# Optimization experiments

Hardware: AMD Instinct MI355X
Metric: run time of the kernel (lower is better)

Reference implementation:

```python
import jax, jax.numpy as jnp
import numpy as np

PI = np.pi
B, NLAT, NLON = 1, 91, 180
DIM, HEADS, DH, KM = 256, 8, 64, 3
DK = DH * KM          # 192: low-rank kernel head dim
LATD = 256            # latent_dim
NK_LONG, NK_LAT = 64, 32


def group_norm(x, g, w, b, eps=1e-5):
    # channel-last GroupNorm: normalize over (spatial..., channels-in-group) per sample
    bsz, C = x.shape[0], x.shape[-1]
    xg = x.reshape(bsz, -1, g, C // g)
    m = xg.mean(axis=(1, 3), keepdims=True)
    v = xg.var(axis=(1, 3), keepdims=True)
    xg = (xg - m) * jax.lax.rsqrt(v + eps)
    return xg.reshape(x.shape) * w + b


def layer_norm(x, w, b, eps=1e-5):
    m = x.mean(-1, keepdims=True)
    v = x.var(-1, keepdims=True)
    return (x - m) * jax.lax.rsqrt(v + eps) * w + b


def gated_mlp(x, w1, b1, w2, b2):
    # MLP([d, d, out], GeAct(GELU)): first linear doubled, gated GELU, then linear
    h = x @ w1 + b1
    c = h.shape[-1] // 2
    return (jax.nn.gelu(h[..., :c]) * h[..., c:]) @ w2 + b2


def pooling_reducer(x, mesh_w, win, lnw, lnb, w1, b1, w2, b2):
    # x: (b, n, m, c); optional mesh weighting along axis 1, mean over axis 2, PreNorm MLP
    x = x @ win
    if mesh_w is not None:
        x = x * mesh_w[None, :, None, None]
    x = x.mean(axis=tuple(range(2, x.ndim - 1)))
    return gated_mlp(layer_norm(x, lnw, lnb), w1, b1, w2, b2)


def bessel_mod(dist, freqs, weight, periodic):
    # radial Bessel basis: sqrt(2/c) * sin(f * d / c) / d, projected to (h, i, j, d)
    if periodic:
        dist = jnp.where(dist > PI, 2.0 * PI - dist, dist)
    d = dist[..., None] + 1e-5
    basis = np.float32(np.sqrt(2.0 / PI)) * jnp.sin(freqs * d / PI) / d  # (i, j, K)
    return jnp.einsum('ijk,khd->hijd', basis, weight)


def latitude_weights(lat, polar_eps=1.0):
    w = jnp.cos(lat)
    dlat = lat[1] - lat[0]
    pw = jnp.sin(dlat / 4.0) ** 2 / jnp.sin(dlat / 2.0)
    w = w.at[0].set(jnp.where(w[0] < 1e-3, polar_eps * pw, w[0]))
    w = w.at[-1].set(jnp.where(w[-1] < 1e-3, polar_eps * pw, w[-1]))
    return jax.lax.stop_gradient(w)  # cached/detached in the torch module


def low_rank_kernel(u_x, u_y, wk, mod):
    # project_qry=False: q is the raw query basis; scaling=1.0; leaky_relu applied outside softmax path
    b, nq, _ = u_x.shape
    nk = u_y.shape[1]
    q = u_x.reshape(b, nq, HEADS, DK).transpose(0, 2, 1, 3)
    k = (u_y @ wk).reshape(b, nk, HEADS, DK).transpose(0, 2, 1, 3)
    K = jnp.einsum('bhid,bhjd,hijd->bhij', q, k, mod)
    return jnp.where(K >= 0, K, 0.2 * K)  # leaky_relu(0.2)


def _forward(u_src, u_lat_qry, u_long_qry, src_lat, src_long, qry_lat, qry_long,
             cm_gn_w, cm_gn_b, cm_w1, cm_b1, cm_w2, cm_b2,
             tl_in_w, tl_ln_w, tl_ln_b, tl_w1, tl_b1, tl_w2, tl_b2,
             ta_in_w, ta_ln_w, ta_ln_b, ta_w1, ta_b1, ta_w2, ta_b2,
             klong_wk, klat_wk,
             pe_long_freq, pe_long_w, pe_lat_freq, pe_lat_w,
             mh_gn_w, mh_gn_b, mh_w):
    # channel mixer: GroupNorm(32) -> Linear -> GELU -> Linear, split into v and u
    u = group_norm(u_src, 32, cm_gn_w, cm_gn_b)
    u = jax.nn.gelu(u @ cm_w1 + cm_b1) @ cm_w2 + cm_b2
    v_src, u_mid = u[..., :HEADS * DH], u[..., HEADS * DH:]

    wlat = latitude_weights(src_lat)
    n_lat_src, n_lon_src = src_lat.shape[-1], src_long.shape[-1]

    # pooled reducers: long pools over lat; lat pools over lon with latitude weights
    u_long_src = pooling_reducer(jnp.swapaxes(u_mid, 1, 2), None,
                                 tl_in_w, tl_ln_w, tl_ln_b, tl_w1, tl_b1, tl_w2, tl_b2)
    u_lat_src = pooling_reducer(u_mid, wlat,
                                ta_in_w, ta_ln_w, ta_ln_b, ta_w1, ta_b1, ta_w2, ta_b2)

    # positional Bessel modulation (cached/detached distances in torch)
    long_dist = jax.lax.stop_gradient(jnp.abs(src_long[None, :] - qry_long[:, None]))
    lat_dist = jax.lax.stop_gradient(jnp.abs(src_lat[None, :] - qry_lat[:, None]))
    mod_long = bessel_mod(long_dist, pe_long_freq, pe_long_w, True)   # (h, lq, ls, DK)
    mod_lat = bessel_mod(lat_dist, pe_lat_freq, pe_lat_w, False)      # (h, iq, is, DK)

    k_long = low_rank_kernel(u_long_qry, u_long_src, klong_wk, mod_long)  # (b,h,lq,ls)
    k_lat = low_rank_kernel(u_lat_qry, u_lat_src, klat_wk, mod_lat)       # (b,h,iq,is)

    b, i, l, _ = v_src.shape
    u_phi = v_src.reshape(b, i, l, HEADS, DH).transpose(0, 3, 1, 2, 4)  # b h i l c
    k_lat = k_lat * wlat[None, None, None, :]
    u_phi = jnp.einsum('bhij,bhjmc->bhimc', k_lat, u_phi) * (PI / n_lat_src)
    u_phi = jnp.einsum('bhlm,bhimc->bhilc', k_long, u_phi) * (2.0 * PI / n_lon_src)
    bq, _, iq, lq, _ = u_phi.shape
    u_phi = u_phi.transpose(0, 2, 3, 1, 4).reshape(bq, iq, lq, HEADS * DH)
    return group_norm(u_phi, HEADS, mh_gn_w, mh_gn_b) @ mh_w


def setup_inputs() -> dict:
    keys = iter(jax.random.split(jax.random.key(0), 48))
    def rn(shape, scale=1.0):
        return jax.random.normal(next(keys), shape, dtype=jnp.float32) * scale
    d = {}
    d['u_src'] = rn((B, NLAT, NLON, DIM))
    d['u_lat_qry'] = rn((B, NLAT, HEADS * DK), 0.1)
    d['u_long_qry'] = rn((B, NLON, HEADS * DK), 0.1)
    lat = jnp.linspace(-PI / 2, PI / 2, NLAT, dtype=jnp.float32)  # includes poles
    lon = jnp.linspace(0.0, 2.0 * PI, NLON, endpoint=False, dtype=jnp.float32)
    d['src_lat'] = lat; d['qry_lat'] = lat
    d['src_long'] = lon; d['qry_long'] = lon
    d['cm_gn_w'] = jnp.ones((DIM,)); d['cm_gn_b'] = jnp.zeros((DIM,))
    d['cm_w1'] = rn((DIM, 4 * DIM), DIM ** -0.5); d['cm_b1'] = jnp.zeros((4 * DIM,))
    d['cm_w2'] = rn((4 * DIM, HEADS * DH + DIM), (4 * DIM) ** -0.5)
    d['cm_b2'] = jnp.zeros((HEADS * DH + DIM,))
    for p in ('tl', 'ta'):
        d[p + '_in_w'] = rn((DIM, DIM), DIM ** -0.5)
        d[p + '_ln_w'] = jnp.ones((DIM,)); d[p + '_ln_b'] = jnp.zeros((DIM,))
        d[p + '_w1'] = rn((DIM, 2 * DIM), DIM ** -0.5); d[p + '_b1'] = jnp.zeros((2 * DIM,))
        d[p + '_w2'] = rn((DIM, LATD), DIM ** -0.5); d[p + '_b2'] = jnp.zeros((LATD,))
    d['klong_wk'] = rn((LATD, HEADS * DK), LATD ** -0.5)
    d['klat_wk'] = rn((LATD, HEADS * DK), LATD ** -0.5)
    d['pe_long_freq'] = PI * jnp.arange(1, NK_LONG + 1, dtype=jnp.float32)
    d['pe_long_w'] = rn((NK_LONG, HEADS, DK), 0.02)
    d['pe_lat_freq'] = PI * jnp.arange(1, NK_LAT + 1, dtype=jnp.float32)
    d['pe_lat_w'] = rn((NK_LAT, HEADS, DK), 0.02)
    d['mh_gn_w'] = jnp.ones((HEADS * DH,)); d['mh_gn_b'] = jnp.zeros((HEADS * DH,))
    d['mh_w'] = rn((HEADS * DH, DIM), (HEADS * DH) ** -0.5)
    return d


def reference(u_src, u_lat_qry, u_long_qry, src_lat, src_long, qry_lat, qry_long,
              cm_gn_w, cm_gn_b, cm_w1, cm_b1, cm_w2, cm_b2,
              tl_in_w, tl_ln_w, tl_ln_b, tl_w1, tl_b1, tl_w2, tl_b2,
              ta_in_w, ta_ln_w, ta_ln_b, ta_w1, ta_b1, ta_w2, ta_b2,
              klong_wk, klat_wk,
              pe_long_freq, pe_long_w, pe_lat_freq, pe_lat_w,
              mh_gn_w, mh_gn_b, mh_w):
    return _forward(u_src, u_lat_qry, u_long_qry, src_lat, src_long, qry_lat, qry_long,
                    cm_gn_w, cm_gn_b, cm_w1, cm_b1, cm_w2, cm_b2,
                    tl_in_w, tl_ln_w, tl_ln_b, tl_w1, tl_b1, tl_w2, tl_b2,
                    ta_in_w, ta_ln_w, ta_ln_b, ta_w1, ta_b1, ta_w2, ta_b2,
                    klong_wk, klat_wk,
                    pe_long_freq, pe_long_w, pe_lat_freq, pe_lat_w,
                    mh_gn_w, mh_gn_b, mh_w)
```

## Files before the change

kernel.cpp:

```cpp
#include <hip/hip_runtime.h>
#include <math.h>

#define PI_F 3.14159265358979323846f

typedef __bf16  bf16x8  __attribute__((ext_vector_type(8)));
typedef float   floatx4 __attribute__((ext_vector_type(4)));

__device__ __forceinline__ float gelu_tanh(float x){
  float x3 = x*x*x;
  float t = tanhf(0.7978845608028654f*(x + 0.044715f*x3));
  return 0.5f*x*(1.0f+t);
}

__device__ __forceinline__ void gl_lds16(const void* g, void* l){
  __builtin_amdgcn_global_load_lds(
      (const __attribute__((address_space(1))) void*)(uintptr_t)g,
      (__attribute__((address_space(3))) void*)(uintptr_t)l,
      16, 0, 0);
}

__global__ __launch_bounds__(256) void prep_k(const float* __restrict__ w2in,
                                              __bf16* __restrict__ wt2,
                                              __bf16* __restrict__ kbuf,
                                              const float* __restrict__ lat,
                                              float* __restrict__ wlat){
  int b = blockIdx.x, t = threadIdx.x;
  if(b < 1440){
    int i = b*256 + t;
    if(i < 368640) kbuf[i] = (__bf16)0.f;
  } else if(b < 4512){
    int idx = (b-1440)*256 + t;
    int n = idx >> 10, k = idx & 1023;
    wt2[idx] = (__bf16)w2in[(size_t)k*768 + n];
  } else {
    if(t < 91) wlat[t] = cosf(lat[t]);
    __syncthreads();
    if(t == 0){
      float dlat = lat[1]-lat[0];
      float s4 = sinf(dlat*0.25f);
      float pw = s4*s4 / sinf(dlat*0.5f);
      if(wlat[0]  < 0.001f) wlat[0]  = pw;
      if(wlat[90] < 0.001f) wlat[90] = pw;
    }
  }
}

__global__ __launch_bounds__(256) void gn1cast_k(const float* __restrict__ x,
                                                 __bf16* __restrict__ xa,
                                                 float* __restrict__ part, int npos){
  int c = threadIdx.x;
  float s=0.f, q=0.f;
  for(int p=blockIdx.x; p<npos; p+=gridDim.x){
    float v = x[p*256 + c];
    xa[p*256 + c] = (__bf16)v;
    s += v; q += v*v;
  }
  __shared__ float ss[256], sq[256];
  ss[c]=s; sq[c]=q;
  __syncthreads();
  if((c&7)==0){
    float a=0.f,b=0.f;
    #pragma unroll
    for(int k=0;k<8;k++){ a+=ss[c+k]; b+=sq[c+k]; }
    int g=c>>3;
    part[(blockIdx.x*32+g)*2+0]=a;
    part[(blockIdx.x*32+g)*2+1]=b;
  }
}

__global__ __launch_bounds__(256) void gn_final_par(const float* __restrict__ part,
                                                    float* __restrict__ stats,
                                                    int nblk, float invN){
  int t = threadIdx.x;
  int g = t & 31, ch = t >> 5;
  float s=0.f,q=0.f;
  for(int b=ch; b<nblk; b+=8){
    s += part[(b*32+g)*2+0];
    q += part[(b*32+g)*2+1];
  }
  __shared__ float ss[256], sq[256];
  ss[t]=s; sq[t]=q;
  __syncthreads();
  if(t<32){
    float a=0.f,bq=0.f;
    #pragma unroll
    for(int c=0;c<8;c++){ a+=ss[c*32+t]; bq+=sq[c*32+t]; }
    float m = a*invN;
    float v = bq*invN - m*m;
    stats[t*2+0]=m;
    stats[t*2+1]=rsqrtf(v+1e-5f);
  }
}

__global__ __launch_bounds__(256) void w1fix_k(const float* __restrict__ w1,
                                               const float* __restrict__ b1,
                                               const float* __restrict__ stats,
                                               const float* __restrict__ gw,
                                               const float* __restrict__ gb,
                                               __bf16* __restrict__ wt1,
                                               float* __restrict__ b1p){
  int n = blockIdx.x, c = threadIdx.x;
  int g = c>>3;
  float m = stats[g*2+0], r = stats[g*2+1];
  float s = r*gw[c];
  float t = gb[c] - m*s;
  float w = w1[(size_t)c*1024 + n];
  wt1[(size_t)n*256 + c] = (__bf16)(s*w);
  __shared__ float red[256];
  red[c] = t*w; __syncthreads();
  for(int st=128; st>0; st>>=1){ if(c<st) red[c]+=red[c+st]; __syncthreads(); }
  if(c==0) b1p[n] = b1[n] + red[0];
}

__global__ __launch_bounds__(256) void w3fix_k(const float* __restrict__ mhw,
                                               const float* __restrict__ part2,
                                               const float* __restrict__ gw,
                                               const float* __restrict__ gb,
                                               __bf16* __restrict__ wt3,
                                               float* __restrict__ b3){
  __shared__ float st[16];
  __shared__ float ps[256], pq[256];
  int n = blockIdx.x, t = threadIdx.x;
  {
    int g = t & 7, ch = t >> 3;
    float s=0.f,q=0.f;
    for(int i=ch; i<91; i+=32){
      s += part2[(g*91+i)*2+0];
      q += part2[(g*91+i)*2+1];
    }
    ps[t]=s; pq[t]=q;
    __syncthreads();
    if(t<8){
      float a=0.f,bq=0.f;
      #pragma unroll
      for(int c=0;c<32;c++){ a+=ps[c*8+t]; bq+=pq[c*8+t]; }
      float m = a*(1.f/1048320.f);
      float v = bq*(1.f/1048320.f) - m*m;
      st[t*2+0]=m; st[t*2+1]=rsqrtf(v+1e-5f);
    }
    __syncthreads();
  }
  float bp=0.f;
  #pragma unroll
  for(int l=0;l<2;l++){
    int cc = t + l*256;
    int g = cc>>6;
    float m = st[g*2+0], r = st[g*2+1];
    float s = r*gw[cc];
    float tt = gb[cc] - m*s;
    float w = mhw[(size_t)cc*256 + n];
    wt3[(size_t)n*512 + cc] = (__bf16)(s*w);
    bp += tt*w;
  }
  __shared__ float red[256];
  red[t]=bp; __syncthreads();
  for(int stp=128;stp>0;stp>>=1){ if(t<stp) red[t]+=red[t+stp]; __syncthreads(); }
  if(t==0) b3[n]=red[0];
}

template<int ACT, int OUTMODE>
__global__ __launch_bounds__(256) void gemm_ld(const __bf16* __restrict__ A,
                                               const __bf16* __restrict__ Bt,
                                               const float* __restrict__ bias,
                                               void* __restrict__ Cp,
                                               __bf16* __restrict__ VB,
                                               __bf16* __restrict__ UM,
                                               int M, int N, int K)
{
  __shared__ __bf16 As[128][32];
  __shared__ __bf16 Bs[128][32];
  const int tid  = threadIdx.x;
  const int lane = tid & 63, wave = tid >> 6;
  const int row0 = blockIdx.x*128, col0 = blockIdx.y*128;
  const int lrow = lane >> 2;
  const int csw  = ((lane&3) ^ ((lane>>3)&3)) * 8;
  const int wr = (wave >> 1)*64, wc = (wave & 1)*64;
  const int m16 = lane & 15, quad = lane >> 4;
  const int pa = (quad ^ ((m16>>1)&3)) * 8;

  const __bf16* Ag0 = A  + (size_t)(row0 + wave*32 + lrow)*K + csw;
  const __bf16* Ag1 = Ag0 + (size_t)16*K;
  const __bf16* Bg0 = Bt + (size_t)(col0 + wave*32 + lrow)*K + csw;
  const __bf16* Bg1 = Bg0 + (size_t)16*K;
  void* la0 = &As[wave*32     ][0];
  void* la1 = &As[wave*32 + 16][0];
  void* lb0 = &Bs[wave*32     ][0];
  void* lb1 = &Bs[wave*32 + 16][0];

  floatx4 acc[4][4];
  #pragma unroll
  for(int i=0;i<4;i++)
    #pragma unroll
    for(int j=0;j<4;j++) acc[i][j] = (floatx4)0.f;

  const int kiters = K >> 5;
  for(int kk=0; kk<kiters; kk++){
    __syncthreads();
    gl_lds16(Ag0, la0);
    gl_lds16(Ag1, la1);
    gl_lds16(Bg0, lb0);
    gl_lds16(Bg1, lb1);
    Ag0 += 32; Ag1 += 32; Bg0 += 32; Bg1 += 32;
    __syncthreads();

    bf16x8 af[4], bfv[4];
    #pragma unroll
    for(int ti=0;ti<4;ti++) af[ti]  = *(const bf16x8*)&As[wr + ti*16 + m16][pa];
    #pragma unroll
    for(int tj=0;tj<4;tj++) bfv[tj] = *(const bf16x8*)&Bs[wc + tj*16 + m16][pa];
    #pragma unroll
    for(int ti=0;ti<4;ti++)
      #pragma unroll
      for(int tj=0;tj<4;tj++)
        acc[ti][tj] = __builtin_amdgcn_mfma_f32_16x16x32_bf16(af[ti], bfv[tj], acc[ti][tj], 0,0,0);
  }

  #pragma unroll
  for(int ti=0;ti<4;ti++){
    #pragma unroll
    for(int reg=0;reg<4;reg++){
      int gr = row0 + wr + ti*16 + quad*4 + reg;
      if(gr >= M) continue;
      int jj = gr/180, mm = gr - jj*180;
      #pragma unroll
      for(int tj=0;tj<4;tj++){
        int gc = col0 + wc + tj*16 + m16;
        float v = acc[ti][tj][reg];
        if(bias) v += bias[gc];
        if(ACT==1) v = gelu_tanh(v);
        if(OUTMODE==2){
          if(gc < 512){
            int hh = gc>>6, cc = gc&63;
            VB[(((size_t)(hh*180+mm)*91)+jj)*64 + cc] = (__bf16)v;
          } else {
            UM[(size_t)gr*256 + (gc-512)] = (__bf16)v;
          }
        } else if(OUTMODE==1){
          ((__bf16*)Cp)[(size_t)gr*N + gc] = (__bf16)v;
        } else {
          ((float*)Cp)[(size_t)gr*N + gc]  = v;
        }
      }
    }
  }
}

__global__ __launch_bounds__(256) void means_k(const __bf16* __restrict__ um,
                                               float* __restrict__ mlon_axis,
                                               float* __restrict__ mlat_axis){
  int b = blockIdx.x, c = threadIdx.x;
  if(b < 180){
    float s=0.f;
    for(int j=0;j<91;j++) s += (float)um[(size_t)(j*180+b)*256 + c];
    mlon_axis[b*256+c] = s*(1.0f/91.0f);
  } else {
    int latr = b-180;
    const __bf16* base = um + (size_t)latr*180*256 + c;
    float s=0.f;
    for(int m=0;m<180;m++) s += (float)base[(size_t)m*256];
    mlat_axis[latr*256+c] = s*(1.0f/180.0f);
  }
}

__device__ __forceinline__ void pool_body(int r, int t,
    const float* __restrict__ x, const float* __restrict__ rs,
    const float* __restrict__ inw,
    const float* __restrict__ lnw, const float* __restrict__ lnb,
    const float* __restrict__ w1, const float* __restrict__ b1,
    const float* __restrict__ w2, const float* __restrict__ b2,
    float* __restrict__ out,
    float* xs, float* xn, float* red, float* g){
  xs[t] = x[r*256+t];
  __syncthreads();
  float y=0.f;
  for(int c=0;c<256;c++) y += xs[c]*inw[c*256+t];
  if(rs) y *= rs[r];
  red[t]=y; __syncthreads();
  for(int s=128;s>0;s>>=1){ if(t<s) red[t]+=red[t+s]; __syncthreads(); }
  float m = red[0]*(1.f/256.f); __syncthreads();
  float d = y-m; red[t]=d*d; __syncthreads();
  for(int s=128;s>0;s>>=1){ if(t<s) red[t]+=red[t+s]; __syncthreads(); }
  float var = red[0]*(1.f/256.f);
  __syncthreads();
  xn[t] = d*rsqrtf(var+1e-5f)*lnw[t]+lnb[t];
  __syncthreads();
  float s1=b1[t], s2=b1[256+t];
  for(int c=0;c<256;c++){ float xv=xn[c]; s1 += xv*w1[c*512+t]; s2 += xv*w1[c*512+256+t]; }
  g[t] = gelu_tanh(s1)*s2;
  __syncthreads();
  float o=b2[t];
  for(int c=0;c<256;c++) o += g[c]*w2[c*256+t];
  out[r*256+t]=o;
}

__global__ __launch_bounds__(256) void pool2_k(
    const float* __restrict__ mlon_axis, const float* __restrict__ mlat_axis,
    const float* __restrict__ wlat,
    const float* __restrict__ tl_inw, const float* __restrict__ tl_lnw, const float* __restrict__ tl_lnb,
    const float* __restrict__ tl_w1, const float* __restrict__ tl_b1,
    const float* __restrict__ tl_w2, const float* __restrict__ tl_b2,
    const float* __restrict__ ta_inw, const float* __restrict__ ta_lnw, const float* __restrict__ ta_lnb,
    const float* __restrict__ ta_w1, const float* __restrict__ ta_b1,
    const float* __restrict__ ta_w2, const float* __restrict__ ta_b2,
    float* __restrict__ ulsrc, float* __restrict__ uasrc){
  __shared__ float xs[256], xn[256], red[256], g[256];
  int b = blockIdx.x, t = threadIdx.x;
  if(b < 180)
    pool_body(b, t, mlon_axis, nullptr, tl_inw, tl_lnw, tl_lnb, tl_w1, tl_b1, tl_w2, tl_b2,
              ulsrc, xs, xn, red, g);
  else
    pool_body(b-180, t, mlat_axis, wlat, ta_inw, ta_lnw, ta_lnb, ta_w1, ta_b1, ta_w2, ta_b2,
              uasrc, xs, xn, red, g);
}

__global__ __launch_bounds__(256) void rowmmT2_k(const float* __restrict__ ulsrc,
                                                 const float* __restrict__ uasrc,
                                                 const float* __restrict__ wlong,
                                                 const float* __restrict__ wlatk,
                                                 float* __restrict__ klkl,
                                                 float* __restrict__ klka){
  int b = blockIdx.x, t = threadIdx.x;
  const float* X; const float* W; float* out; int r, R;
  if(b < 180){ r=b;     X=ulsrc; W=wlong; out=klkl; R=180; }
  else       { r=b-180; X=uasrc; W=wlatk; out=klka; R=91;  }
  int j = blockIdx.y*256 + t;
  __shared__ float xs[256];
  xs[t] = X[r*256 + t];
  __syncthreads();
  float s = 0.f;
  for(int c=0;c<256;c++) s += xs[c]*W[(size_t)c*1536 + j];
  out[(size_t)j*R + r] = s;
}

__global__ __launch_bounds__(256) void modu2_k(const float* __restrict__ lon,
                                               const float* __restrict__ lat,
                                               const float* __restrict__ flong,
                                               const float* __restrict__ flat,
                                               const float* __restrict__ wlong,
                                               const float* __restrict__ wlatm,
                                               float* __restrict__ modul,
                                               float* __restrict__ modua){
  int b = blockIdx.x, t = threadIdx.x;
  const float* coord; const float* freqs; const float* W; float* out;
  int h, m, nm, nk, periodic;
  if(b < 1440){ h=b/180; m=b%180; nm=180; nk=64; periodic=1; coord=lon; freqs=flong; W=wlong; out=modul; }
  else        { int b2=b-1440; h=b2/91; m=b2%91; nm=91; nk=32; periodic=0; coord=lat; freqs=flat; W=wlatm; out=modua; }
  __shared__ float basis[64];
  float dist = fabsf(coord[m] - coord[0]);
  if(periodic && dist > PI_F) dist = 2.f*PI_F - dist;
  float d = dist + 1e-5f;
  if(t < nk) basis[t] = 0.7978845608028654f * sinf(freqs[t]*d/PI_F) / d;
  __syncthreads();
  if(t < 192){
    float s=0.f;
    for(int k=0;k<nk;k++) s += basis[k]*W[(size_t)(k*8+h)*192+t];
    out[((size_t)h*192 + t)*nm + m] = s;
  }
}

__global__ __launch_bounds__(256) void lrk2_k(const float* __restrict__ qlong,
                                              const float* __restrict__ qlat,
                                              const float* __restrict__ klkl,
                                              const float* __restrict__ klka,
                                              const float* __restrict__ modul,
                                              const float* __restrict__ modua,
                                              const float* __restrict__ wlat,
                                              __bf16* __restrict__ kbg,
                                              __bf16* __restrict__ kbl){
  int b = blockIdx.x, t = threadIdx.x;
  const float* qry; const float* kt; const float* mt; const float* js; __bf16* out;
  int h, i, n, pitch; float scale;
  if(b < 1440){ h=b/180; i=b%180; n=180; pitch=192; qry=qlong; kt=klkl; mt=modul; js=nullptr; out=kbg; scale=2.f*PI_F/180.f; }
  else        { int b2=b-1440; h=b2/91; i=b2%91; n=91; pitch=96; qry=qlat; kt=klka; mt=modua; js=wlat; out=kbl; scale=PI_F/91.f; }
  __shared__ float qs[192];
  if(t<192) qs[t] = qry[(size_t)i*1536 + h*192 + t];
  __syncthreads();
  int j = t;
  if(j < n){
    int m = abs(i-j);
    const float* kp = kt + (size_t)h*192*n;
    const float* mp = mt + (size_t)h*192*n;
    float s=0.f;
    #pragma unroll 4
    for(int d=0;d<192;d++) s += qs[d] * kp[(size_t)d*n + j] * mp[(size_t)d*n + m];
    s = (s>=0.f) ? s : 0.2f*s;
    if(js) s *= js[j];
    out[((size_t)h*pitch + i)*pitch + j] = (__bf16)(s*scale);
  }
}

__global__ __launch_bounds__(256) void apply1_mfma(const __bf16* __restrict__ Kl,
                                                   const __bf16* __restrict__ vbf,
                                                   __bf16* __restrict__ u1){
  int h = blockIdx.x / 180, m = blockIdx.x % 180;
  __shared__ __bf16 vst[64][104];
  int t = threadIdx.x;
  const __bf16* src = vbf + ((size_t)(h*180+m)*91)*64;
  for(int idx=t; idx<91*64; idx+=256){
    int j = idx>>6, c = idx&63;
    vst[c][j] = src[idx];
  }
  for(int idx=t; idx<64*13; idx+=256){
    int c = idx/13, j = 91 + idx - (idx/13)*13;
    vst[c][j] = (__bf16)0.f;
  }
  __syncthreads();
  int lane = t & 63, wave = t>>6;
  int m16 = lane & 15, quad = lane>>4;
  floatx4 acc[6];
  #pragma unroll
  for(int i=0;i<6;i++) acc[i]=(floatx4)0.f;
  const __bf16* Ab = Kl + (size_t)h*96*96;
  #pragma unroll
  for(int kc=0; kc<3; kc++){
    bf16x8 bfrag = *(const bf16x8*)&vst[wave*16 + m16][kc*32 + quad*8];
    #pragma unroll
    for(int ti=0;ti<6;ti++){
      bf16x8 afrag = *(const bf16x8*)&Ab[(size_t)(ti*16+m16)*96 + kc*32 + quad*8];
      acc[ti] = __builtin_amdgcn_mfma_f32_16x16x32_bf16(afrag, bfrag, acc[ti], 0,0,0);
    }
  }
  #pragma unroll
  for(int ti=0;ti<6;ti++){
    #pragma unroll
    for(int reg=0;reg<4;reg++){
      int i = ti*16 + quad*4 + reg;
      if(i<91){
        int c = wave*16 + m16;
        u1[(((size_t)(h*91+i)*180)+m)*64 + c] = (__bf16)acc[ti][reg];
      }
    }
  }
}

__global__ __launch_bounds__(256) void apply2_mfma(const __bf16* __restrict__ Kg,
                                                   const __bf16* __restrict__ u1,
                                                   __bf16* __restrict__ a2,
                                                   float* __restrict__ part2){
  int h = blockIdx.x / 91, i = blockIdx.x % 91;
  __shared__ __bf16 vst[64][208];
  __shared__ float rs[256], rq[256];
  int t = threadIdx.x;
  const __bf16* src = u1 + ((size_t)(h*91+i)*180)*64;
  for(int idx=t; idx<180*64; idx+=256){
    int m = idx>>6, c = idx&63;
    vst[c][m] = src[idx];
  }
  for(int idx=t; idx<64*28; idx+=256){
    int c = idx/28, m = 180 + idx - (idx/28)*28;
    vst[c][m] = (__bf16)0.f;
  }
  __syncthreads();
  int lane = t&63, wave = t>>6;
  int m16 = lane&15, quad = lane>>4;
  floatx4 acc[12];
  #pragma unroll
  for(int l=0;l<12;l++) acc[l]=(floatx4)0.f;
  const __bf16* Ab = Kg + (size_t)h*192*192;
  for(int kc=0; kc<6; kc++){
    bf16x8 bfrag = *(const bf16x8*)&vst[wave*16+m16][kc*32 + quad*8];
    #pragma unroll
    for(int tl=0; tl<12; tl++){
      bf16x8 afrag = *(const bf16x8*)&Ab[(size_t)(tl*16+m16)*192 + kc*32 + quad*8];
      acc[tl] = __builtin_amdgcn_mfma_f32_16x16x32_bf16(afrag, bfrag, acc[tl], 0,0,0);
    }
  }
  float s=0.f, q=0.f;
  #pragma unroll
  for(int tl=0; tl<12; tl++){
    #pragma unroll
    for(int reg=0; reg<4; reg++){
      int l = tl*16 + quad*4 + reg;
      if(l<180){
        int c = wave*16+m16;
        float v = acc[tl][reg];
        a2[((size_t)i*180 + l)*512 + h*64 + c] = (__bf16)v;
        s += v; q += v*v;
      }
    }
  }
  rs[t]=s; rq[t]=q;
  __syncthreads();
  for(int st=128; st>0; st>>=1){ if(t<st){ rs[t]+=rs[t+st]; rq[t]+=rq[t+st]; } __syncthreads(); }
  if(t==0){ part2[blockIdx.x*2+0]=rs[0]; part2[blockIdx.x*2+1]=rq[0]; }
}

extern "C" void kernel_launch(void* const* d_in, const int* in_sizes, int n_in,
                              void* d_out, int out_size, void* d_ws, size_t ws_size,
                              hipStream_t stream){
  const float* u_src      = (const float*)d_in[0];
  const float* u_lat_qry  = (const float*)d_in[1];
  const float* u_long_qry = (const float*)d_in[2];
  const float* lat = (const float*)d_in[3];
  const float* lon = (const float*)((in_sizes[4]==180)? d_in[4] : d_in[5]);
  const float* cm_gn_w = (const float*)d_in[7];
  const float* cm_gn_b = (const float*)d_in[8];
  const float* cm_w1   = (const float*)d_in[9];
  const float* cm_b1   = (const float*)d_in[10];
  const float* cm_w2   = (const float*)d_in[11];
  const float* cm_b2   = (const float*)d_in[12];
  const float* tl_in_w = (const float*)d_in[13];
  const float* tl_ln_w = (const float*)d_in[14];
  const float* tl_ln_b = (const float*)d_in[15];
  const float* tl_w1   = (const float*)d_in[16];
  const float* tl_b1   = (const float*)d_in[17];
  const float* tl_w2   = (const float*)d_in[18];
  const float* tl_b2   = (const float*)d_in[19];
  const float* ta_in_w = (const float*)d_in[20];
  const float* ta_ln_w = (const float*)d_in[21];
  const float* ta_ln_b = (const float*)d_in[22];
  const float* ta_w1   = (const float*)d_in[23];
  const float* ta_b1   = (const float*)d_in[24];
  const float* ta_w2   = (const float*)d_in[25];
  const float* ta_b2   = (const float*)d_in[26];
  const float* klong_wk= (const float*)d_in[27];
  const float* klat_wk = (const float*)d_in[28];
  const float* pe_long_freq = (const float*)d_in[29];
  const float* pe_long_w    = (const float*)d_in[30];
  const float* pe_lat_freq  = (const float*)d_in[31];
  const float* pe_lat_w     = (const float*)d_in[32];
  const float* mh_gn_w = (const float*)d_in[33];
  const float* mh_gn_b = (const float*)d_in[34];
  const float* mh_w    = (const float*)d_in[35];

  float* ws = (float*)d_ws;
  const size_t OFF_PART1  = 0;
  const size_t OFF_GN1    = 32768;
  const size_t OFF_WLAT   = 32896;
  const size_t OFF_MEANLON= 33024;
  const size_t OFF_MEANLAT= 79104;
  const size_t OFF_ULSRC  = 102400;
  const size_t OFF_UASRC  = 148480;
  const size_t OFF_KLKL   = 171776;
  const size_t OFF_KLKA   = 448256;
  const size_t OFF_MODUL  = 588032;
  const size_t OFF_MODUA  = 864512;
  const size_t OFF_KBL    = 1004288;
  const size_t OFF_KBG    = 1041152;
  const size_t OFF_PART2  = 1188608;
  const size_t OFF_B1P    = 1190064;
  const size_t OFF_B3     = 1191088;
  const size_t OFF_WT1    = 1191424;
  const size_t OFF_WT2    = 1322496;
  const size_t OFF_WT3    = 1715712;
  const size_t OFF_VBF    = 1781248;
  const size_t OFF_A2     = 1781248;
  const size_t OFF_UMID   = 5974528;
  const size_t OFF_H1     = 8071168;
  const size_t OFF_U1     = 8071168;
  const size_t OFF_A1     = 16457728;

  const int NPOS = 16380;

  prep_k<<<4513,256,0,stream>>>(cm_w2, (__bf16*)(ws+OFF_WT2), (__bf16*)(ws+OFF_KBL),
      lat, ws+OFF_WLAT);

  gn1cast_k<<<512,256,0,stream>>>(u_src, (__bf16*)(ws+OFF_A1), ws+OFF_PART1, NPOS);
  gn_final_par<<<1,256,0,stream>>>(ws+OFF_PART1, ws+OFF_GN1, 512, 1.f/131040.f);

  w1fix_k<<<1024,256,0,stream>>>(cm_w1, cm_b1, ws+OFF_GN1, cm_gn_w, cm_gn_b,
      (__bf16*)(ws+OFF_WT1), ws+OFF_B1P);

  gemm_ld<1,1><<<dim3(128,8),256,0,stream>>>((const __bf16*)(ws+OFF_A1),
      (const __bf16*)(ws+OFF_WT1), ws+OFF_B1P, ws+OFF_H1, nullptr, nullptr, NPOS, 1024, 256);

  gemm_ld<0,2><<<dim3(128,6),256,0,stream>>>((const __bf16*)(ws+OFF_H1),
      (const __bf16*)(ws+OFF_WT2), cm_b2, nullptr, (__bf16*)(ws+OFF_VBF),
      (__bf16*)(ws+OFF_UMID), NPOS, 768, 1024);

  means_k<<<271,256,0,stream>>>((const __bf16*)(ws+OFF_UMID), ws+OFF_MEANLON, ws+OFF_MEANLAT);

  pool2_k<<<271,256,0,stream>>>(ws+OFF_MEANLON, ws+OFF_MEANLAT, ws+OFF_WLAT,
      tl_in_w, tl_ln_w, tl_ln_b, tl_w1, tl_b1, tl_w2, tl_b2,
      ta_in_w, ta_ln_w, ta_ln_b, ta_w1, ta_b1, ta_w2, ta_b2,
      ws+OFF_ULSRC, ws+OFF_UASRC);

  rowmmT2_k<<<dim3(271,6),256,0,stream>>>(ws+OFF_ULSRC, ws+OFF_UASRC, klong_wk, klat_wk,
      ws+OFF_KLKL, ws+OFF_KLKA);

  modu2_k<<<2168,256,0,stream>>>(lon, lat, pe_long_freq, pe_lat_freq, pe_long_w, pe_lat_w,
      ws+OFF_MODUL, ws+OFF_MODUA);

  lrk2_k<<<2168,256,0,stream>>>(u_long_qry, u_lat_qry, ws+OFF_KLKL, ws+OFF_KLKA,
      ws+OFF_MODUL, ws+OFF_MODUA, ws+OFF_WLAT, (__bf16*)(ws+OFF_KBG), (__bf16*)(ws+OFF_KBL));

  apply1_mfma<<<8*180,256,0,stream>>>((const __bf16*)(ws+OFF_KBL), (const __bf16*)(ws+OFF_VBF),
      (__bf16*)(ws+OFF_U1));
  apply2_mfma<<<8*91, 256,0,stream>>>((const __bf16*)(ws+OFF_KBG), (const __bf16*)(ws+OFF_U1),
      (__bf16*)(ws+OFF_A2), ws+OFF_PART2);

  w3fix_k<<<256,256,0,stream>>>(mh_w, ws+OFF_PART2, mh_gn_w, mh_gn_b,
      (__bf16*)(ws+OFF_WT3), ws+OFF_B3);
  gemm_ld<0,0><<<dim3(128,2),256,0,stream>>>((const __bf16*)(ws+OFF_A2),
      (const __bf16*)(ws+OFF_WT3), ws+OFF_B3, (float*)d_out, nullptr, nullptr, NPOS, 256, 512);
}
```

Measured before the change: 448.9 us.

## Deepen GEMM K-tile, fuse means into pooling, stage apply outputs via LDS

The bf16 GEMM now loads a 64-wide K slice per iteration with an 8-way XOR swizzle and runs two MFMA sub-steps, which halves the number of barrier-separated load phases. The separate means kernel is merged into the pooling kernel, removing one launch and the intermediate mean buffers. The apply1 and apply2 kernels now stage their outputs in shared memory and write 16-byte vectors to global memory instead of scattered 2-byte stores. The cost is more LDS use per GEMM block and extra barriers in the apply kernels.

```diff
diff --git a/kernel.cpp b/kernel.cpp
--- a/kernel.cpp
+++ b/kernel.cpp
@@ -167,25 +167,18 @@
                                                __bf16* __restrict__ UM,
                                                int M, int N, int K)
 {
-  __shared__ __bf16 As[128][32];
-  __shared__ __bf16 Bs[128][32];
+  __shared__ __bf16 As[128][64];
+  __shared__ __bf16 Bs[128][64];
   const int tid  = threadIdx.x;
   const int lane = tid & 63, wave = tid >> 6;
   const int row0 = blockIdx.x*128, col0 = blockIdx.y*128;
-  const int lrow = lane >> 2;
-  const int csw  = ((lane&3) ^ ((lane>>3)&3)) * 8;
+  const int lrow = lane >> 3;
+  const int csw  = ((lane&7) ^ (lrow&7)) * 8;
   const int wr = (wave >> 1)*64, wc = (wave & 1)*64;
   const int m16 = lane & 15, quad = lane >> 4;
-  const int pa = (quad ^ ((m16>>1)&3)) * 8;
-
-  const __bf16* Ag0 = A  + (size_t)(row0 + wave*32 + lrow)*K + csw;
-  const __bf16* Ag1 = Ag0 + (size_t)16*K;
-  const __bf16* Bg0 = Bt + (size_t)(col0 + wave*32 + lrow)*K + csw;
-  const __bf16* Bg1 = Bg0 + (size_t)16*K;
-  void* la0 = &As[wave*32     ][0];
-  void* la1 = &As[wave*32 + 16][0];
-  void* lb0 = &Bs[wave*32     ][0];
-  void* lb1 = &Bs[wave*32 + 16][0];
+
+  const __bf16* Ag = A  + (size_t)(row0 + wave*32 + lrow)*K + csw;
+  const __bf16* Bg = Bt + (size_t)(col0 + wave*32 + lrow)*K + csw;
 
   floatx4 acc[4][4];
   #pragma unroll
@@ -193,26 +186,31 @@
     #pragma unroll
     for(int j=0;j<4;j++) acc[i][j] = (floatx4)0.f;
 
-  const int kiters = K >> 5;
+  const int kiters = K >> 6;
   for(int kk=0; kk<kiters; kk++){
     __syncthreads();
-    gl_lds16(Ag0, la0);
-    gl_lds16(Ag1, la1);
-    gl_lds16(Bg0, lb0);
-    gl_lds16(Bg1, lb1);
-    Ag0 += 32; Ag1 += 32; Bg0 += 32; Bg1 += 32;
-    __syncthreads();
-
-    bf16x8 af[4], bfv[4];
-    #pragma unroll
-    for(int ti=0;ti<4;ti++) af[ti]  = *(const bf16x8*)&As[wr + ti*16 + m16][pa];
-    #pragma unroll
-    for(int tj=0;tj<4;tj++) bfv[tj] = *(const bf16x8*)&Bs[wc + tj*16 + m16][pa];
-    #pragma unroll
-    for(int ti=0;ti<4;ti++)
+    #pragma unroll
+    for(int L=0;L<4;L++){
+      gl_lds16(Ag + (size_t)(L*8)*K, &As[wave*32 + L*8][0]);
+      gl_lds16(Bg + (size_t)(L*8)*K, &Bs[wave*32 + L*8][0]);
+    }
+    Ag += 64; Bg += 64;
+    __syncthreads();
+
+    #pragma unroll
+    for(int sub=0; sub<2; sub++){
+      const int pa = (((sub<<2)+quad) ^ (m16&7)) << 3;
+      bf16x8 af[4], bfv[4];
       #pragma unroll
-      for(int tj=0;tj<4;tj++)
-        acc[ti][tj] = __builtin_amdgcn_mfma_f32_16x16x32_bf16(af[ti], bfv[tj], acc[ti][tj], 0,0,0);
+      for(int ti=0;ti<4;ti++) af[ti]  = *(const bf16x8*)&As[wr + ti*16 + m16][pa];
+      #pragma unroll
+      for(int tj=0;tj<4;tj++) bfv[tj] = *(const bf16x8*)&Bs[wc + tj*16 + m16][pa];
+      #pragma unroll
+      for(int ti=0;ti<4;ti++)
+        #pragma unroll
+        for(int tj=0;tj<4;tj++)
+          acc[ti][tj] = __builtin_amdgcn_mfma_f32_16x16x32_bf16(af[ti], bfv[tj], acc[ti][tj], 0,0,0);
+    }
   }
 
   #pragma unroll
@@ -245,36 +243,12 @@
   }
 }
 
-__global__ __launch_bounds__(256) void means_k(const __bf16* __restrict__ um,
-                                               float* __restrict__ mlon_axis,
-                                               float* __restrict__ mlat_axis){
-  int b = blockIdx.x, c = threadIdx.x;
-  if(b < 180){
-    float s=0.f;
-    for(int j=0;j<91;j++) s += (float)um[(size_t)(j*180+b)*256 + c];
-    mlon_axis[b*256+c] = s*(1.0f/91.0f);
-  } else {
-    int latr = b-180;
-    const __bf16* base = um + (size_t)latr*180*256 + c;
-    float s=0.f;
-    for(int m=0;m<180;m++) s += (float)base[(size_t)m*256];
-    mlat_axis[latr*256+c] = s*(1.0f/180.0f);
-  }
-}
-
-__device__ __forceinline__ void pool_body(int r, int t,
-    const float* __restrict__ x, const float* __restrict__ rs,
-    const float* __restrict__ inw,
+__device__ __forceinline__ void pool_core(int r, int t, float y,
     const float* __restrict__ lnw, const float* __restrict__ lnb,
     const float* __restrict__ w1, const float* __restrict__ b1,
     const float* __restrict__ w2, const float* __restrict__ b2,
     float* __restrict__ out,
-    float* xs, float* xn, float* red, float* g){
-  xs[t] = x[r*256+t];
-  __syncthreads();
-  float y=0.f;
-  for(int c=0;c<256;c++) y += xs[c]*inw[c*256+t];
-  if(rs) y *= rs[r];
+    float* xn, float* red, float* g){
   red[t]=y; __syncthreads();
   for(int s=128;s>0;s>>=1){ if(t<s) red[t]+=red[t+s]; __syncthreads(); }
   float m = red[0]*(1.f/256.f); __syncthreads();
@@ -293,9 +267,8 @@
   out[r*256+t]=o;
 }
 
-__global__ __launch_bounds__(256) void pool2_k(
-    const float* __restrict__ mlon_axis, const float* __restrict__ mlat_axis,
-    const float* __restrict__ wlat,
+__global__ __launch_bounds__(256) void mpool_k(
+    const __bf16* __restrict__ um, const float* __restrict__ wlat,
     const float* __restrict__ tl_inw, const float* __restrict__ tl_lnw, const float* __restrict__ tl_lnb,
     const float* __restrict__ tl_w1, const float* __restrict__ tl_b1,
     const float* __restrict__ tl_w2, const float* __restrict__ tl_b2,
@@ -305,12 +278,26 @@
     float* __restrict__ ulsrc, float* __restrict__ uasrc){
   __shared__ float xs[256], xn[256], red[256], g[256];
   int b = blockIdx.x, t = threadIdx.x;
-  if(b < 180)
-    pool_body(b, t, mlon_axis, nullptr, tl_inw, tl_lnw, tl_lnb, tl_w1, tl_b1, tl_w2, tl_b2,
-              ulsrc, xs, xn, red, g);
-  else
-    pool_body(b-180, t, mlat_axis, wlat, ta_inw, ta_lnw, ta_lnb, ta_w1, ta_b1, ta_w2, ta_b2,
-              uasrc, xs, xn, red, g);
+  if(b < 180){
+    float s=0.f;
+    for(int j=0;j<91;j++) s += (float)um[(size_t)(j*180+b)*256 + t];
+    xs[t] = s*(1.0f/91.0f);
+    __syncthreads();
+    float y=0.f;
+    for(int c=0;c<256;c++) y += xs[c]*tl_inw[c*256+t];
+    pool_core(b, t, y, tl_lnw, tl_lnb, tl_w1, tl_b1, tl_w2, tl_b2, ulsrc, xn, red, g);
+  } else {
+    int r = b-180;
+    const __bf16* base = um + (size_t)r*180*256 + t;
+    float s=0.f;
+    for(int m=0;m<180;m++) s += (float)base[(size_t)m*256];
+    xs[t] = s*(1.0f/180.0f);
+    __syncthreads();
+    float y=0.f;
+    for(int c=0;c<256;c++) y += xs[c]*ta_inw[c*256+t];
+    y *= wlat[r];
+    pool_core(r, t, y, ta_lnw, ta_lnb, ta_w1, ta_b1, ta_w2, ta_b2, uasrc, xn, red, g);
+  }
 }
 
 __global__ __launch_bounds__(256) void rowmmT2_k(const float* __restrict__ ulsrc,
@@ -420,16 +407,22 @@
       acc[ti] = __builtin_amdgcn_mfma_f32_16x16x32_bf16(afrag, bfrag, acc[ti], 0,0,0);
     }
   }
+  __syncthreads();
+  __bf16* ost = &vst[0][0];
+  int c = wave*16 + m16;
   #pragma unroll
   for(int ti=0;ti<6;ti++){
     #pragma unroll
     for(int reg=0;reg<4;reg++){
       int i = ti*16 + quad*4 + reg;
-      if(i<91){
-        int c = wave*16 + m16;
-        u1[(((size_t)(h*91+i)*180)+m)*64 + c] = (__bf16)acc[ti][reg];
-      }
-    }
+      if(i<91) ost[i*72 + c] = (__bf16)acc[ti][reg];
+    }
+  }
+  __syncthreads();
+  __bf16* dst = u1 + (((size_t)(h*91)*180)+m)*64;
+  for(int idx=t; idx<91*8; idx+=256){
+    int i = idx>>3, cc = idx&7;
+    *(bf16x8*)(dst + (size_t)i*180*64 + cc*8) = *(const bf16x8*)&ost[i*72 + cc*8];
   }
 }
 
@@ -465,6 +458,9 @@
       acc[tl] = __builtin_amdgcn_mfma_f32_16x16x32_bf16(afrag, bfrag, acc[tl], 0,0,0);
     }
   }
+  __syncthreads();
+  __bf16* ost = &vst[0][0];
+  int c = wave*16+m16;
   float s=0.f, q=0.f;
   #pragma unroll
   for(int tl=0; tl<12; tl++){
@@ -472,9 +468,8 @@
     for(int reg=0; reg<4; reg++){
       int l = tl*16 + quad*4 + reg;
       if(l<180){
-        int c = wave*16+m16;
         float v = acc[tl][reg];
-        a2[((size_t)i*180 + l)*512 + h*64 + c] = (__bf16)v;
+        ost[l*72 + c] = (__bf16)v;
         s += v; q += v*v;
       }
     }
@@ -483,6 +478,11 @@
   __syncthreads();
   for(int st=128; st>0; st>>=1){ if(t<st){ rs[t]+=rs[t+st]; rq[t]+=rq[t+st]; } __syncthreads(); }
   if(t==0){ part2[blockIdx.x*2+0]=rs[0]; part2[blockIdx.x*2+1]=rq[0]; }
+  __bf16* dst = a2 + (size_t)i*180*512 + h*64;
+  for(int idx=t; idx<180*8; idx+=256){
+    int l = idx>>3, cc = idx&7;
+    *(bf16x8*)(dst + (size_t)l*512 + cc*8) = *(const bf16x8*)&ost[l*72 + cc*8];
+  }
 }
 
 extern "C" void kernel_launch(void* const* d_in, const int* in_sizes, int n_in,
@@ -527,28 +527,26 @@
   const size_t OFF_PART1  = 0;
   const size_t OFF_GN1    = 32768;
   const size_t OFF_WLAT   = 32896;
-  const size_t OFF_MEANLON= 33024;
-  const size_t OFF_MEANLAT= 79104;
-  const size_t OFF_ULSRC  = 102400;
-  const size_t OFF_UASRC  = 148480;
-  const size_t OFF_KLKL   = 171776;
-  const size_t OFF_KLKA   = 448256;
-  const size_t OFF_MODUL  = 588032;
-  const size_t OFF_MODUA  = 864512;
-  const size_t OFF_KBL    = 1004288;
-  const size_t OFF_KBG    = 1041152;
-  const size_t OFF_PART2  = 1188608;
-  const size_t OFF_B1P    = 1190064;
-  const size_t OFF_B3     = 1191088;
-  const size_t OFF_WT1    = 1191424;
-  const size_t OFF_WT2    = 1322496;
-  const size_t OFF_WT3    = 1715712;
-  const size_t OFF_VBF    = 1781248;
-  const size_t OFF_A2     = 1781248;
-  const size_t OFF_UMID   = 5974528;
-  const size_t OFF_H1     = 8071168;
-  const size_t OFF_U1     = 8071168;
-  const size_t OFF_A1     = 16457728;
+  const size_t OFF_ULSRC  = 33024;
+  const size_t OFF_UASRC  = 79104;
+  const size_t OFF_KLKL   = 102400;
+  const size_t OFF_KLKA   = 378880;
+  const size_t OFF_MODUL  = 518656;
+  const size_t OFF_MODUA  = 795136;
+  const size_t OFF_KBL    = 934912;
+  const size_t OFF_KBG    = 971776;
+  const size_t OFF_PART2  = 1119232;
+  const size_t OFF_B1P    = 1120688;
+  const size_t OFF_B3     = 1121712;
+  const size_t OFF_WT1    = 1122048;
+  const size_t OFF_WT2    = 1253120;
+  const size_t OFF_WT3    = 1646336;
+  const size_t OFF_VBF    = 1711872;
+  const size_t OFF_A2     = 1711872;
+  const size_t OFF_UMID   = 5905152;
+  const size_t OFF_H1     = 8001792;
+  const size_t OFF_U1     = 8001792;
+  const size_t OFF_A1     = 16388352;
 
   const int NPOS = 16380;
 
@@ -568,9 +566,7 @@
       (const __bf16*)(ws+OFF_WT2), cm_b2, nullptr, (__bf16*)(ws+OFF_VBF),
       (__bf16*)(ws+OFF_UMID), NPOS, 768, 1024);
 
-  means_k<<<271,256,0,stream>>>((const __bf16*)(ws+OFF_UMID), ws+OFF_MEANLON, ws+OFF_MEANLAT);
-
-  pool2_k<<<271,256,0,stream>>>(ws+OFF_MEANLON, ws+OFF_MEANLAT, ws+OFF_WLAT,
+  mpool_k<<<271,256,0,stream>>>((const __bf16*)(ws+OFF_UMID), ws+OFF_WLAT,
       tl_in_w, tl_ln_w, tl_ln_b, tl_w1, tl_b1, tl_w2, tl_b2,
       ta_in_w, ta_ln_w, ta_ln_b, ta_w1, ta_b1, ta_w2, ta_b2,
       ws+OFF_ULSRC, ws+OFF_UASRC);
```

New measurement: 454.9 us. No clear change (+1.3%).
